# Optimization experiments

Measured on AMD Instinct MI355X. Metric: run time of the kernel, lower is better.

Reference implementation:

```python
import jax, jax.numpy as jnp
import numpy as np

WS = 8        # window_size
NH = 8        # num_heads
LN_EPS = 1e-5

# static relative-position index table [WS*WS, WS*WS], values in [0, (2*WS-1)**2)
def _rel_index(ws):
    coords = np.arange(ws)
    grid = np.stack(np.meshgrid(coords, coords, indexing='ij')).reshape(2, -1)  # [2, W2]
    rel = grid[:, :, None] - grid[:, None, :]            # [2, W2, W2]
    rel = rel.transpose(1, 2, 0).copy()                   # [W2, W2, 2]
    rel[..., 0] += ws - 1
    rel[..., 1] += ws - 1
    rel[..., 0] *= 2 * ws - 1
    return rel.sum(-1)                                    # [W2, W2]

REL_IDX = jnp.asarray(_rel_index(WS))


def _ln(x):
    # LayerNorm without affine params (elementwise_affine=False)
    mu = jnp.mean(x, axis=-1, keepdims=True)
    var = jnp.var(x, axis=-1, keepdims=True)
    return (x - mu) * jax.lax.rsqrt(var + LN_EPS)


def setup_inputs() -> dict:
    key = jax.random.key(0)
    ks = jax.random.split(key, 16)
    B, Hg, Wg, C = 8, 64, 64, 256
    L = Hg * Wg
    s = 0.02
    inp = {
        'x': jax.random.normal(ks[0], (B, L, C), jnp.float32),
        't_embed': jax.random.normal(ks[1], (B, C), jnp.float32),
        'H': Hg,
        'W': Wg,
        'adaln1_w': s * jax.random.normal(ks[2], (C, 2 * C), jnp.float32),
        'adaln1_b': jnp.zeros((2 * C,), jnp.float32),
        'adaln2_w': s * jax.random.normal(ks[3], (C, 2 * C), jnp.float32),
        'adaln2_b': jnp.zeros((2 * C,), jnp.float32),
        'bias_table': s * jax.random.normal(ks[4], ((2 * WS - 1) ** 2, NH), jnp.float32),
        'q_w': s * jax.random.normal(ks[5], (C, C), jnp.float32),
        'q_b': jnp.zeros((C,), jnp.float32),
        'k_w': s * jax.random.normal(ks[6], (C, C), jnp.float32),
        'k_b': jnp.zeros((C,), jnp.float32),
        'v_w': s * jax.random.normal(ks[7], (C, C), jnp.float32),
        'v_b': jnp.zeros((C,), jnp.float32),
        'o_w': s * jax.random.normal(ks[8], (C, C), jnp.float32),
        'o_b': jnp.zeros((C,), jnp.float32),
        'ffn1_w': s * jax.random.normal(ks[9], (C, 4 * C), jnp.float32),
        'ffn1_b': jnp.zeros((4 * C,), jnp.float32),
        'ffn2_w': s * jax.random.normal(ks[10], (4 * C, C), jnp.float32),
        'ffn2_b': jnp.zeros((C,), jnp.float32),
    }
    return inp


def reference(x, t_embed, H, W, adaln1_w, adaln1_b, adaln2_w, adaln2_b,
              bias_table, q_w, q_b, k_w, k_b, v_w, v_b, o_w, o_b,
              ffn1_w, ffn1_b, ffn2_w, ffn2_b):
    B, L, C = x.shape
    d = C // NH
    W2 = WS * WS
    sh = WS // 2  # cyclic shift (shifted=True)

    # --- AdaLN1 ---
    ss = t_embed @ adaln1_w + adaln1_b              # [B, 2C]
    scale, shift = jnp.split(ss, 2, axis=-1)
    xn = _ln(x) * (1.0 + scale[:, None, :]) + shift[:, None, :]

    # --- shifted window partition ---
    xg = xn.reshape(B, H, W, C)
    xg = jnp.roll(xg, (-sh, -sh), axis=(1, 2))
    xw = xg.reshape(B, H // WS, WS, W // WS, WS, C).transpose(0, 1, 3, 2, 4, 5)
    xw = xw.reshape(-1, W2, C)                       # [nwB, W2, C]
    nwB = xw.shape[0]

    # --- window attention with relative position bias ---
    q = (xw @ q_w + q_b).reshape(nwB, W2, NH, d).transpose(0, 2, 1, 3)
    k = (xw @ k_w + k_b).reshape(nwB, W2, NH, d).transpose(0, 2, 1, 3)
    v = (xw @ v_w + v_b).reshape(nwB, W2, NH, d).transpose(0, 2, 1, 3)
    logits = jnp.einsum('whqd,whkd->whqk', q, k) * (d ** -0.5)
    bias = bias_table[REL_IDX.reshape(-1)].reshape(W2, W2, NH).transpose(2, 0, 1)
    logits = logits + bias[None].astype(logits.dtype)
    attn = jax.nn.softmax(logits, axis=-1)
    out = jnp.einsum('whqk,whkd->whqd', attn, v).transpose(0, 2, 1, 3).reshape(nwB, W2, C)
    out = out @ o_w + o_b

    # --- window reverse + unshift ---
    xm = out.reshape(B, H // WS, W // WS, WS, WS, C).transpose(0, 1, 3, 2, 4, 5)
    xm = xm.reshape(B, H, W, C)
    xm = jnp.roll(xm, (sh, sh), axis=(1, 2))
    x = x + xm.reshape(B, L, C)

    # --- AdaLN2 + FFN (GELU exact, matching torch nn.GELU) ---
    ss2 = t_embed @ adaln2_w + adaln2_b
    sc2, sh2 = jnp.split(ss2, 2, axis=-1)
    xn2 = _ln(x) * (1.0 + sc2[:, None, :]) + sh2[:, None, :]
    h = jax.nn.gelu(xn2 @ ffn1_w + ffn1_b, approximate=False)
    x = x + (h @ ffn2_w + ffn2_b)
    return x
```

## Files before the change

kernel.cpp:

```cpp
#include <hip/hip_runtime.h>
#include <math.h>

#define WS_ 8
#define NH_ 8
#define C_ 256
#define B_ 8
#define M_ 32768
#define SH_ 4
#define LN_EPS 1e-5f
#define SL_ 8388608

typedef __attribute__((ext_vector_type(8))) short bf16x8;
typedef __attribute__((ext_vector_type(4))) float f32x4;

__device__ inline float b2f(unsigned short u) {
    union { unsigned int i; float f; } c; c.i = ((unsigned int)u) << 16; return c.f;
}
__device__ inline unsigned short f2b(float f) {
    union { unsigned int i; float f; } c; c.f = f;
    unsigned int u = c.i;
    return (unsigned short)((u + 0x7FFFu + ((u >> 16) & 1u)) >> 16);
}
__device__ inline float gelu_f(float x) {
    float t = 1.59576912160573f * (x + 0.044715f * x * x * x);
    return x / (1.f + __expf(-t));
}

__global__ void prep_k(const float* __restrict__ qw, const float* __restrict__ kw,
                       const float* __restrict__ vw, const float* __restrict__ ow,
                       const float* __restrict__ f1w, const float* __restrict__ f2w,
                       const float* __restrict__ qb, const float* __restrict__ kb,
                       const float* __restrict__ vb, const float* __restrict__ bt,
                       const float* __restrict__ te,
                       const float* __restrict__ a1w, const float* __restrict__ a1b,
                       const float* __restrict__ a2w, const float* __restrict__ a2b,
                       unsigned short* __restrict__ qkvT, unsigned short* __restrict__ oT,
                       unsigned short* __restrict__ f1T, unsigned short* __restrict__ f2T,
                       float* __restrict__ qkvB, float* __restrict__ bias_full,
                       float* __restrict__ ss1, float* __restrict__ ss2) {
    int t = blockIdx.x * 256 + threadIdx.x;
    if (t < 196608) {
        int n = t >> 8, k = t & 255;
        const float* w = n < 256 ? qw : (n < 512 ? kw : vw);
        qkvT[t] = f2b(w[k * 256 + (n & 255)]);
    } else if (t < 262144) {
        int i = t - 196608; int n = i >> 8, k = i & 255;
        oT[i] = f2b(ow[k * 256 + n]);
    } else if (t < 524288) {
        int i = t - 262144; int n = i >> 8, k = i & 255;
        f1T[i] = f2b(f1w[k * 1024 + n]);
    } else if (t < 786432) {
        int i = t - 524288; int n = i >> 10, k = i & 1023;
        f2T[i] = f2b(f2w[k * 256 + n]);
    } else if (t < 787200) {
        int i = t - 786432;
        qkvB[i] = i < 256 ? qb[i] : (i < 512 ? kb[i - 256] : vb[i - 512]);
    } else if (t < 819968) {
        int i = t - 787200;
        int head = i >> 12, qk = i & 4095;
        int q = qk >> 6, k = qk & 63;
        int qh = q >> 3, qw2 = q & 7, kh = k >> 3, kw2 = k & 7;
        bias_full[i] = bt[((qh - kh + 7) * 15 + (qw2 - kw2 + 7)) * 8 + head];
    } else if (t < 828160) {
        int i = t - 819968;
        int which = i >> 12;
        int rem = i & 4095;
        int b = rem >> 9, col = rem & 511;
        const float* w = which ? a2w : a1w;
        const float* bb = which ? a2b : a1b;
        const float* tr = te + b * C_;
        float acc = bb[col];
        for (int k = 0; k < C_; ++k) acc += tr[k] * w[k * 512 + col];
        (which ? ss2 : ss1)[b * 512 + col] = acc;
    }
}

__global__ __launch_bounds__(256) void ln_win_k(const float* __restrict__ x,
                                                const float* __restrict__ ss,
                                                unsigned short* __restrict__ xw) {
    int t = blockIdx.x * 4 + (threadIdx.x >> 6);
    int lane = threadIdx.x & 63;
    int b = t >> 12, rem = t & 4095;
    int hg = rem >> 6, wg = rem & 63;
    int hs = (hg + SH_) & 63, wsrc = (wg + SH_) & 63;
    size_t src = ((size_t)b << 12) + (hs << 6) + wsrc;
    float4 v = *(const float4*)&x[src * C_ + lane * 4];
    float s = v.x + v.y + v.z + v.w;
    float s2 = v.x * v.x + v.y * v.y + v.z * v.z + v.w * v.w;
#pragma unroll
    for (int m = 1; m < 64; m <<= 1) { s += __shfl_xor(s, m); s2 += __shfl_xor(s2, m); }
    float mu = s * (1.f / 256.f);
    float rstd = rsqrtf(s2 * (1.f / 256.f) - mu * mu + LN_EPS);
    float4 sc = *(const float4*)&ss[b * 512 + lane * 4];
    float4 sh = *(const float4*)&ss[b * 512 + 256 + lane * 4];
    int win = (b << 6) + ((hg >> 3) << 3) + (wg >> 3);
    int pos = ((hg & 7) << 3) + (wg & 7);
    ushort4 pk;
    pk.x = f2b((v.x - mu) * rstd * (1.f + sc.x) + sh.x);
    pk.y = f2b((v.y - mu) * rstd * (1.f + sc.y) + sh.y);
    pk.z = f2b((v.z - mu) * rstd * (1.f + sc.z) + sh.z);
    pk.w = f2b((v.w - mu) * rstd * (1.f + sc.w) + sh.w);
    *(ushort4*)(xw + (size_t)(win * 64 + pos) * C_ + lane * 4) = pk;
}

template <int KDIM, int MODE, int NT, int MINW>
__global__ __launch_bounds__(256, MINW) void gemm_bf16_k(
    const unsigned short* __restrict__ A, const unsigned short* __restrict__ Bt,
    const float* __restrict__ bias, const float* __restrict__ res,
    void* __restrict__ Cout, int Nout) {
    __shared__ __align__(16) unsigned short smem[16384];
    unsigned short (*As)[4096] = (unsigned short (*)[4096])&smem[0];
    unsigned short (*Bs)[4096] = (unsigned short (*)[4096])&smem[8192];
    const int blk = blockIdx.x;
    const int xcd = blk & 7;
    const int idx = blk >> 3;
    const int mt = xcd + ((idx / NT) << 3);
    const int nt = idx % NT;
    const int bm = mt * 128, bn = nt * 128;
    const int tid = threadIdx.x;
    const int w = tid >> 6, lane = tid & 63;
    const int quad = lane >> 4, l16 = lane & 15;
    const int wm = (w >> 1) * 64, wn = (w & 1) * 64;
    const int srow = lane >> 2;
    const int qlog = ((lane & 3) ^ ((lane >> 3) & 3)) << 3;
    const int rsw = ((l16 >> 1) & 3) << 3;

    f32x4 acc[4][4] = {};

    for (int k0 = 0; k0 < KDIM; k0 += 64) {
        if (k0) __syncthreads();
#pragma unroll
        for (int h = 0; h < 2; ++h) {
#pragma unroll
            for (int j = 0; j < 2; ++j) {
                int r = j * 64 + w * 16 + srow;
                const unsigned short* ga = A + (size_t)(bm + r) * KDIM + k0 + h * 32 + qlog;
                unsigned short* la = &As[h][j * 2048 + w * 512 + lane * 8];
                __builtin_amdgcn_global_load_lds(
                    (const __attribute__((address_space(1))) void*)ga,
                    (__attribute__((address_space(3))) void*)la, 16, 0, 0);
                const unsigned short* gb = Bt + (size_t)(bn + r) * KDIM + k0 + h * 32 + qlog;
                unsigned short* lb = &Bs[h][j * 2048 + w * 512 + lane * 8];
                __builtin_amdgcn_global_load_lds(
                    (const __attribute__((address_space(1))) void*)gb,
                    (__attribute__((address_space(3))) void*)lb, 16, 0, 0);
            }
        }
        __syncthreads();
#pragma unroll
        for (int h = 0; h < 2; ++h) {
            bf16x8 af[4], bfr[4];
#pragma unroll
            for (int i = 0; i < 4; ++i)
                af[i] = *(const bf16x8*)&As[h][(wm + i * 16 + l16) * 32 + ((quad << 3) ^ rsw)];
#pragma unroll
            for (int j = 0; j < 4; ++j)
                bfr[j] = *(const bf16x8*)&Bs[h][(wn + j * 16 + l16) * 32 + ((quad << 3) ^ rsw)];
#pragma unroll
            for (int i = 0; i < 4; ++i)
#pragma unroll
                for (int j = 0; j < 4; ++j)
                    acc[i][j] = __builtin_amdgcn_mfma_f32_16x16x32_bf16(
                        bfr[j], af[i], acc[i][j], 0, 0, 0);
        }
    }

    if constexpr (MODE == 0 || MODE == 2) {
        __syncthreads();
#pragma unroll
        for (int i = 0; i < 4; ++i) {
            const int lrow = wm + i * 16 + l16;
#pragma unroll
            for (int j = 0; j < 4; ++j) {
                const int lcol = wn + j * 16 + quad * 4;
                float4 bv = *(const float4*)&bias[bn + lcol];
                float v0 = acc[i][j][0] + bv.x, v1 = acc[i][j][1] + bv.y;
                float v2 = acc[i][j][2] + bv.z, v3 = acc[i][j][3] + bv.w;
                ushort4 pk;
                if (MODE == 2) {
                    pk.x = f2b(gelu_f(v0)); pk.y = f2b(gelu_f(v1));
                    pk.z = f2b(gelu_f(v2)); pk.w = f2b(gelu_f(v3));
                } else {
                    pk.x = f2b(v0); pk.y = f2b(v1); pk.z = f2b(v2); pk.w = f2b(v3);
                }
                int sw = (lcol >> 3) ^ (lrow & 7);
                *(ushort4*)&smem[lrow * 128 + sw * 8 + (lcol & 7)] = pk;
            }
        }
        __syncthreads();
#pragma unroll
        for (int p = 0; p < 8; ++p) {
            const int lrow = p * 16 + (tid >> 4);
            const int c16 = tid & 15;
            bf16x8 v = *(const bf16x8*)&smem[lrow * 128 + ((c16 ^ (lrow & 7)) * 8)];
            const int grow = bm + lrow;
            if (MODE == 2) {
                *(bf16x8*)((unsigned short*)Cout + (size_t)grow * Nout + bn + c16 * 8) = v;
            } else {
                int win = grow >> 6, pos = grow & 63;
                int col = bn + c16 * 8;
                int which = col >> 8, head = (col >> 5) & 7, dc = col & 31;
                *(bf16x8*)((unsigned short*)Cout + (size_t)which * SL_ +
                           (size_t)win * 16384 + pos * 32 + head * 2048 + dc) = v;
            }
        }
    } else {
#pragma unroll
        for (int i = 0; i < 4; ++i) {
            const int row = bm + wm + i * 16 + l16;
            size_t rowbase = (size_t)row * Nout;
#pragma unroll
            for (int j = 0; j < 4; ++j) {
                const int col = bn + wn + j * 16 + quad * 4;
                float4 bv = *(const float4*)&bias[col];
                float v0 = acc[i][j][0] + bv.x, v1 = acc[i][j][1] + bv.y;
                float v2 = acc[i][j][2] + bv.z, v3 = acc[i][j][3] + bv.w;
                float4 rv = *(const float4*)&res[rowbase + col];
                float4 ov = {v0 + rv.x, v1 + rv.y, v2 + rv.z, v3 + rv.w};
                *(float4*)&((float*)Cout)[rowbase + col] = ov;
            }
        }
    }
}

__global__ __launch_bounds__(512, 2) void oproj_ln_k(
    const unsigned short* __restrict__ A, const unsigned short* __restrict__ Bt,
    const float* __restrict__ bias, const float* __restrict__ res,
    float* __restrict__ x1, const float* __restrict__ ss2,
    unsigned short* __restrict__ xn2) {
    __shared__ __align__(16) unsigned short As[4][128 * 32];
    __shared__ __align__(16) unsigned short Bs[4][256 * 32];
    const int bm = blockIdx.x * 128;
    const int tid = threadIdx.x;
    const int w = tid >> 6, lane = tid & 63;
    const int quad = lane >> 4, l16 = lane & 15;
    const int wrow = (w >> 2) * 64, wcol = (w & 3) * 64;
    const int rsw = ((l16 >> 1) & 3) << 3;
    const int srow = tid >> 2;
    const int gch = ((tid & 3) ^ ((srow >> 1) & 3)) << 3;

    f32x4 acc[4][4] = {};

    for (int k0 = 0; k0 < 256; k0 += 128) {
        if (k0) __syncthreads();
#pragma unroll
        for (int h = 0; h < 4; ++h) {
            const unsigned short* ga = A + (size_t)(bm + srow) * 256 + k0 + h * 32 + gch;
            __builtin_amdgcn_global_load_lds(
                (const __attribute__((address_space(1))) void*)ga,
                (__attribute__((address_space(3))) void*)&As[h][tid * 8], 16, 0, 0);
#pragma unroll
            for (int s = 0; s < 2; ++s) {
                const unsigned short* gb = Bt + (size_t)(s * 128 + srow) * 256 + k0 + h * 32 + gch;
                __builtin_amdgcn_global_load_lds(
                    (const __attribute__((address_space(1))) void*)gb,
                    (__attribute__((address_space(3))) void*)&Bs[h][s * 4096 + tid * 8], 16, 0, 0);
            }
        }
        __syncthreads();
#pragma unroll
        for (int h = 0; h < 4; ++h) {
            bf16x8 af[4], bfr[4];
#pragma unroll
            for (int i = 0; i < 4; ++i)
                af[i] = *(const bf16x8*)&As[h][(wrow + i * 16 + l16) * 32 + ((quad << 3) ^ rsw)];
#pragma unroll
            for (int j = 0; j < 4; ++j)
                bfr[j] = *(const bf16x8*)&Bs[h][(wcol + j * 16 + l16) * 32 + ((quad << 3) ^ rsw)];
#pragma unroll
            for (int i = 0; i < 4; ++i)
#pragma unroll
                for (int j = 0; j < 4; ++j)
                    acc[i][j] = __builtin_amdgcn_mfma_f32_16x16x32_bf16(
                        bfr[j], af[i], acc[i][j], 0, 0, 0);
        }
    }

    float ps[4], ps2[4];
#pragma unroll
    for (int i = 0; i < 4; ++i) {
        const int row = bm + wrow + i * 16 + l16;
        int win = row >> 6, pos = row & 63;
        int b = win >> 6, wh = (win >> 3) & 7, ww = win & 7;
        int hg = (wh << 3) + (pos >> 3), wg = (ww << 3) + (pos & 7);
        int hd = (hg + SH_) & 63, wd = (wg + SH_) & 63;
        size_t rowbase = (((size_t)b << 12) + (hd << 6) + wd) * C_;
        float s = 0.f, s2 = 0.f;
#pragma unroll
        for (int j = 0; j < 4; ++j) {
            const int col = wcol + j * 16 + quad * 4;
            float4 bv = *(const float4*)&bias[col];
            float4 rv = *(const float4*)&res[rowbase + col];
            float4 ov = {acc[i][j][0] + bv.x + rv.x, acc[i][j][1] + bv.y + rv.y,
                         acc[i][j][2] + bv.z + rv.z, acc[i][j][3] + bv.w + rv.w};
            *(float4*)&x1[rowbase + col] = ov;
            acc[i][j][0] = ov.x; acc[i][j][1] = ov.y;
            acc[i][j][2] = ov.z; acc[i][j][3] = ov.w;
            s += ov.x + ov.y + ov.z + ov.w;
            s2 += ov.x * ov.x + ov.y * ov.y + ov.z * ov.z + ov.w * ov.w;
        }
        ps[i] = s; ps2[i] = s2;
    }
#pragma unroll
    for (int i = 0; i < 4; ++i) {
        ps[i] += __shfl_xor(ps[i], 16);  ps[i] += __shfl_xor(ps[i], 32);
        ps2[i] += __shfl_xor(ps2[i], 16); ps2[i] += __shfl_xor(ps2[i], 32);
    }
    float* sred = (float*)&As[0][0];
    __syncthreads();
    if (quad == 0) {
#pragma unroll
        for (int i = 0; i < 4; ++i) {
            int r = i * 16 + l16;
            sred[(w * 64 + r) * 2 + 0] = ps[i];
            sred[(w * 64 + r) * 2 + 1] = ps2[i];
        }
    }
    __syncthreads();
#pragma unroll
    for (int i = 0; i < 4; ++i) {
        int r = i * 16 + l16;
        float s = 0.f, s2 = 0.f;
#pragma unroll
        for (int cw = 0; cw < 4; ++cw) {
            s  += sred[(((w >> 2) * 4 + cw) * 64 + r) * 2 + 0];
            s2 += sred[(((w >> 2) * 4 + cw) * 64 + r) * 2 + 1];
        }
        float mu = s * (1.f / 256.f);
        float rstd = rsqrtf(s2 * (1.f / 256.f) - mu * mu + LN_EPS);
        const int row = bm + wrow + i * 16 + l16;
        int win = row >> 6, pos = row & 63;
        int b = win >> 6, wh = (win >> 3) & 7, ww = win & 7;
        int hg = (wh << 3) + (pos >> 3), wg = (ww << 3) + (pos & 7);
        int hd = (hg + SH_) & 63, wd = (wg + SH_) & 63;
        size_t rowbase = (((size_t)b << 12) + (hd << 6) + wd) * C_;
#pragma unroll
        for (int j = 0; j < 4; ++j) {
            const int col = wcol + j * 16 + quad * 4;
            float4 scv = *(const float4*)&ss2[b * 512 + col];
            float4 shv = *(const float4*)&ss2[b * 512 + 256 + col];
            ushort4 pk;
            pk.x = f2b((acc[i][j][0] - mu) * rstd * (1.f + scv.x) + shv.x);
            pk.y = f2b((acc[i][j][1] - mu) * rstd * (1.f + scv.y) + shv.y);
            pk.z = f2b((acc[i][j][2] - mu) * rstd * (1.f + scv.z) + shv.z);
            pk.w = f2b((acc[i][j][3] - mu) * rstd * (1.f + scv.w) + shv.w);
            *(ushort4*)(xn2 + rowbase + col) = pk;
        }
    }
}

__global__ __launch_bounds__(256) void attn_mfma_k(
    const unsigned short* __restrict__ qkv, const float* __restrict__ bias_full,
    unsigned short* __restrict__ attn_out) {
    __shared__ __align__(16) unsigned short Pb[4][64 * 66];
    __shared__ __align__(16) unsigned short Vt[4][32 * 66];
    const int w = threadIdx.x >> 6, lane = threadIdx.x & 63;
    const int wh = blockIdx.x * 4 + w;
    const int win = wh >> 3, head = wh & 7;
    const int quad = lane >> 4, l16 = lane & 15;

    const unsigned short* qp = qkv + (size_t)win * 16384 + head * 2048;
    const unsigned short* kp = qp + SL_;
    const unsigned short* vp = qp + 2 * (size_t)SL_;

    {
        const uint4* v4 = (const uint4*)(vp + lane * 32);
        unsigned short* dst = &Vt[w][0];
#pragma unroll
        for (int c = 0; c < 4; ++c) {
            uint4 u = v4[c];
            unsigned int uu[4] = {u.x, u.y, u.z, u.w};
#pragma unroll
            for (int p = 0; p < 4; ++p) {
                int d0 = c * 8 + p * 2;
                dst[d0 * 66 + lane] = (unsigned short)(uu[p] & 0xffff);
                dst[(d0 + 1) * 66 + lane] = (unsigned short)(uu[p] >> 16);
            }
        }
    }

    bf16x8 qf[4], kf[4];
#pragma unroll
    for (int i = 0; i < 4; ++i) {
        qf[i] = *(const bf16x8*)(qp + (i * 16 + l16) * 32 + quad * 8);
        kf[i] = *(const bf16x8*)(kp + (i * 16 + l16) * 32 + quad * 8);
    }

    f32x4 s[4][4] = {};
#pragma unroll
    for (int i = 0; i < 4; ++i)
#pragma unroll
        for (int j = 0; j < 4; ++j)
            s[i][j] = __builtin_amdgcn_mfma_f32_16x16x32_bf16(qf[i], kf[j], s[i][j], 0, 0, 0);

    const float scale = 0.17677669529663687f;
    const float* bf = bias_full + head * 4096;
    float rs[4][4];
#pragma unroll
    for (int i = 0; i < 4; ++i) {
#pragma unroll
        for (int r = 0; r < 4; ++r) {
            int row = i * 16 + quad * 4 + r;
            float acc = 0.f;
#pragma unroll
            for (int j = 0; j < 4; ++j) {
                float e = __expf(s[i][j][r] * scale + bf[row * 64 + j * 16 + l16]);
                s[i][j][r] = e;
                acc += e;
            }
#pragma unroll
            for (int msk = 1; msk < 16; msk <<= 1) acc += __shfl_xor(acc, msk);
            rs[i][r] = 1.f / acc;
        }
    }

#pragma unroll
    for (int i = 0; i < 4; ++i)
#pragma unroll
        for (int j = 0; j < 4; ++j)
#pragma unroll
            for (int r = 0; r < 4; ++r)
                Pb[w][(i * 16 + quad * 4 + r) * 66 + j * 16 + l16] = f2b(s[i][j][r]);

    __syncthreads();

    f32x4 o[4][2] = {};
#pragma unroll
    for (int st = 0; st < 2; ++st) {
        bf16x8 bv[2];
#pragma unroll
        for (int jo = 0; jo < 2; ++jo)
            bv[jo] = *(const bf16x8*)&Vt[w][(jo * 16 + l16) * 66 + st * 32 + quad * 8];
#pragma unroll
        for (int i = 0; i < 4; ++i) {
            bf16x8 af = *(const bf16x8*)&Pb[w][(i * 16 + l16) * 66 + st * 32 + quad * 8];
#pragma unroll
            for (int jo = 0; jo < 2; ++jo)
                o[i][jo] = __builtin_amdgcn_mfma_f32_16x16x32_bf16(af, bv[jo], o[i][jo], 0, 0, 0);
        }
    }

#pragma unroll
    for (int i = 0; i < 4; ++i)
#pragma unroll
        for (int jo = 0; jo < 2; ++jo)
#pragma unroll
            for (int r = 0; r < 4; ++r) {
                int row = i * 16 + quad * 4 + r;
                int d = jo * 16 + l16;
                attn_out[((size_t)(win * 64 + row)) * C_ + head * 32 + d] =
                    f2b(o[i][jo][r] * rs[i][r]);
            }
}

extern "C" void kernel_launch(void* const* d_in, const int* in_sizes, int n_in,
                              void* d_out, int out_size, void* d_ws, size_t ws_size,
                              hipStream_t stream) {
    const float* x        = (const float*)d_in[0];
    const float* t_embed  = (const float*)d_in[1];
    const float* adaln1_w = (const float*)d_in[4];
    const float* adaln1_b = (const float*)d_in[5];
    const float* adaln2_w = (const float*)d_in[6];
    const float* adaln2_b = (const float*)d_in[7];
    const float* bt       = (const float*)d_in[8];
    const float* q_w = (const float*)d_in[9],  *q_b = (const float*)d_in[10];
    const float* k_w = (const float*)d_in[11], *k_b = (const float*)d_in[12];
    const float* v_w = (const float*)d_in[13], *v_b = (const float*)d_in[14];
    const float* o_w = (const float*)d_in[15], *o_b = (const float*)d_in[16];
    const float* f1_w = (const float*)d_in[17], *f1_b = (const float*)d_in[18];
    const float* f2_w = (const float*)d_in[19], *f2_b = (const float*)d_in[20];
    float* out = (float*)d_out;

    char* wsb = (char*)d_ws;
    float* ss1            = (float*)(wsb + 0);
    float* ss2            = (float*)(wsb + 16384);
    float* qkvB           = (float*)(wsb + 32768);
    unsigned short* qkvT  = (unsigned short*)(wsb + 36864);
    unsigned short* oT    = (unsigned short*)(wsb + 430080);
    unsigned short* f1T   = (unsigned short*)(wsb + 561152);
    unsigned short* f2T   = (unsigned short*)(wsb + 1085440);
    float* bias_full      = (float*)(wsb + 1609728);
    unsigned short* xw    = (unsigned short*)(wsb + 2097152);
    unsigned short* qkv   = (unsigned short*)(wsb + 18874368);
    unsigned short* attn  = (unsigned short*)(wsb + 69206016);
    unsigned short* xn2   = xw;
    unsigned short* hbuf  = qkv;
    float* x1             = (float*)(wsb + 85983232);

    prep_k<<<3235, 256, 0, stream>>>(q_w, k_w, v_w, o_w, f1_w, f2_w, q_b, k_b, v_b, bt,
                                     t_embed, adaln1_w, adaln1_b, adaln2_w, adaln2_b,
                                     qkvT, oT, f1T, f2T, qkvB, bias_full, ss1, ss2);
    ln_win_k<<<8192, 256, 0, stream>>>(x, ss1, xw);

    gemm_bf16_k<256, 0, 6, 3><<<1536, 256, 0, stream>>>(xw, qkvT, qkvB, nullptr, qkv, 768);

    attn_mfma_k<<<1024, 256, 0, stream>>>(qkv, bias_full, attn);

    oproj_ln_k<<<256, 512, 0, stream>>>(attn, oT, o_b, x, x1, ss2, xn2);

    gemm_bf16_k<256, 2, 8, 3><<<2048, 256, 0, stream>>>(xn2, f1T, f1_b, nullptr, hbuf, 1024);
    gemm_bf16_k<1024, 3, 2, 1><<<512, 256, 0, stream>>>(hbuf, f2T, f2_b, x1, out, 256);
}
```

Before: 261.9 us.

## Fuse FFN1, GELU and FFN2 into one kernel keeping hidden activations in LDS

Replaces the two FFN GEMM launches with one kernel. Each block takes a 64-row tile and computes the hidden layer in four 256-wide chunks. Each chunk goes through GELU into swizzled shared memory and is consumed right away by the second GEMM, accumulating in registers. This removes the round trip of the 32768x1024 bf16 hidden tensor through global memory and one launch. In exchange, B weight fragments are read straight from global or L2 without LDS staging, and only 512 blocks are launched, which may limit occupancy.

New measurement: 268.6 us. 1.03x slower.

```diff
diff --git a/kernel.cpp b/kernel.cpp
--- a/kernel.cpp
+++ b/kernel.cpp
@@ -349,6 +349,113 @@
     }
 }
 
+__global__ __launch_bounds__(512, 4) void ffn_fused_k(
+    const unsigned short* __restrict__ xn2, const unsigned short* __restrict__ f1T,
+    const unsigned short* __restrict__ f2T, const float* __restrict__ f1b,
+    const float* __restrict__ f2bias, const float* __restrict__ x1,
+    float* __restrict__ out) {
+    __shared__ __align__(16) unsigned short Ahs[8][2048];
+    __shared__ __align__(16) unsigned short hs[64 * 256];
+    const int tid = threadIdx.x;
+    const int w = tid >> 6, lane = tid & 63;
+    const int quad = lane >> 4, l16 = lane & 15;
+    const int brow = blockIdx.x * 64;
+    const int rsw = ((l16 >> 1) & 3) << 3;
+
+    if (tid < 256) {
+        const int arow = tid >> 2;
+        const int qa = ((tid & 3) ^ ((tid >> 3) & 3)) << 3;
+#pragma unroll
+        for (int h = 0; h < 8; ++h) {
+            const unsigned short* ga = xn2 + (size_t)(brow + arow) * 256 + h * 32 + qa;
+            __builtin_amdgcn_global_load_lds(
+                (const __attribute__((address_space(1))) void*)ga,
+                (__attribute__((address_space(3))) void*)&Ahs[h][tid * 8], 16, 0, 0);
+        }
+    }
+    f32x4 acc2[4][2] = {};
+    __syncthreads();
+
+    for (int c = 0; c < 4; ++c) {
+        f32x4 a1[4][2] = {};
+        const unsigned short* bp1 =
+            f1T + (size_t)(c * 256 + w * 32 + l16) * 256 + quad * 8;
+#pragma unroll
+        for (int k8 = 0; k8 < 8; ++k8) {
+            bf16x8 ax[4], bf[2];
+#pragma unroll
+            for (int j = 0; j < 2; ++j)
+                bf[j] = *(const bf16x8*)(bp1 + (size_t)j * 16 * 256 + k8 * 32);
+#pragma unroll
+            for (int i = 0; i < 4; ++i)
+                ax[i] = *(const bf16x8*)&Ahs[k8][(i * 16 + l16) * 32 + ((quad << 3) ^ rsw)];
+            __builtin_amdgcn_s_setprio(1);
+#pragma unroll
+            for (int i = 0; i < 4; ++i)
+#pragma unroll
+                for (int j = 0; j < 2; ++j)
+                    a1[i][j] = __builtin_amdgcn_mfma_f32_16x16x32_bf16(
+                        bf[j], ax[i], a1[i][j], 0, 0, 0);
+            __builtin_amdgcn_s_setprio(0);
+        }
+        if (c) __syncthreads();
+#pragma unroll
+        for (int i = 0; i < 4; ++i) {
+            int row = i * 16 + l16;
+#pragma unroll
+            for (int j = 0; j < 2; ++j) {
+                int hl = w * 32 + j * 16 + quad * 4;
+                float4 bv = *(const float4*)&f1b[c * 256 + hl];
+                ushort4 pk;
+                pk.x = f2b(gelu_f(a1[i][j][0] + bv.x));
+                pk.y = f2b(gelu_f(a1[i][j][1] + bv.y));
+                pk.z = f2b(gelu_f(a1[i][j][2] + bv.z));
+                pk.w = f2b(gelu_f(a1[i][j][3] + bv.w));
+                int ch = hl >> 3, half = (hl >> 2) & 1;
+                *(ushort4*)&hs[row * 256 + ((ch ^ (row & 7)) << 3) + half * 4] = pk;
+            }
+        }
+        __syncthreads();
+        const unsigned short* bp2 =
+            f2T + (size_t)(w * 32 + l16) * 1024 + c * 256 + quad * 8;
+#pragma unroll
+        for (int k8 = 0; k8 < 8; ++k8) {
+            bf16x8 ah[4], bg[2];
+#pragma unroll
+            for (int jo = 0; jo < 2; ++jo)
+                bg[jo] = *(const bf16x8*)(bp2 + (size_t)jo * 16 * 1024 + k8 * 32);
+#pragma unroll
+            for (int i = 0; i < 4; ++i) {
+                int row = i * 16 + l16;
+                int ch = (k8 * 4 + quad) ^ (row & 7);
+                ah[i] = *(const bf16x8*)&hs[row * 256 + ch * 8];
+            }
+            __builtin_amdgcn_s_setprio(1);
+#pragma unroll
+            for (int i = 0; i < 4; ++i)
+#pragma unroll
+                for (int jo = 0; jo < 2; ++jo)
+                    acc2[i][jo] = __builtin_amdgcn_mfma_f32_16x16x32_bf16(
+                        bg[jo], ah[i], acc2[i][jo], 0, 0, 0);
+            __builtin_amdgcn_s_setprio(0);
+        }
+    }
+
+#pragma unroll
+    for (int i = 0; i < 4; ++i) {
+        int row = brow + i * 16 + l16;
+#pragma unroll
+        for (int jo = 0; jo < 2; ++jo) {
+            int col = w * 32 + jo * 16 + quad * 4;
+            float4 bv = *(const float4*)&f2bias[col];
+            float4 rv = *(const float4*)&x1[(size_t)row * 256 + col];
+            float4 ov = {acc2[i][jo][0] + bv.x + rv.x, acc2[i][jo][1] + bv.y + rv.y,
+                         acc2[i][jo][2] + bv.z + rv.z, acc2[i][jo][3] + bv.w + rv.w};
+            *(float4*)&out[(size_t)row * 256 + col] = ov;
+        }
+    }
+}
+
 __global__ __launch_bounds__(256) void attn_mfma_k(
     const unsigned short* __restrict__ qkv, const float* __restrict__ bias_full,
     unsigned short* __restrict__ attn_out) {
@@ -484,7 +591,6 @@
     unsigned short* qkv   = (unsigned short*)(wsb + 18874368);
     unsigned short* attn  = (unsigned short*)(wsb + 69206016);
     unsigned short* xn2   = xw;
-    unsigned short* hbuf  = qkv;
     float* x1             = (float*)(wsb + 85983232);
 
     prep_k<<<3235, 256, 0, stream>>>(q_w, k_w, v_w, o_w, f1_w, f2_w, q_b, k_b, v_b, bt,
@@ -498,6 +604,5 @@
 
     oproj_ln_k<<<256, 512, 0, stream>>>(attn, oT, o_b, x, x1, ss2, xn2);
 
-    gemm_bf16_k<256, 2, 8, 3><<<2048, 256, 0, stream>>>(xn2, f1T, f1_b, nullptr, hbuf, 1024);
-    gemm_bf16_k<1024, 3, 2, 1><<<512, 256, 0, stream>>>(hbuf, f2T, f2_b, x1, out, 256);
-}
+    ffn_fused_k<<<512, 512, 0, stream>>>(xn2, f1T, f2T, f1_b, f2_b, x1, out);
+}
```

## Keep full-K A tile resident in LDS across multiple N tiles for QKV and FFN1 GEMMs

Applied to the files above, without the earlier changes.

Adds a new GEMM kernel that loads a 128x256 A tile into LDS once and sweeps several 128-wide N tiles, streaming only B in 64-wide K slices. It replaces the QKV and FFN1 GEMM launches, cutting repeated global reads of A and launching fewer, larger (512-thread) blocks. The epilogue stages output through LDS for coalesced writes. The trade-offs are 80KB of LDS per block, which lowers occupancy, and a load/sync per K slice with no double buffering.

After: 264.6 us. About the same (+1.0%).

```diff
diff --git a/kernel.cpp b/kernel.cpp
--- a/kernel.cpp
+++ b/kernel.cpp
@@ -103,6 +103,124 @@
     *(ushort4*)(xw + (size_t)(win * 64 + pos) * C_ + lane * 4) = pk;
 }
 
+template <int MODE, int NTB>
+__global__ __launch_bounds__(512, 4) void gemm_pa_k(
+    const unsigned short* __restrict__ A, const unsigned short* __restrict__ Bt,
+    const float* __restrict__ bias, void* __restrict__ Cout, int Nout) {
+    __shared__ __align__(16) unsigned short As[128 * 256];
+    __shared__ __align__(16) unsigned short Bs[128 * 64];
+    const int blk = blockIdx.x;
+    const int mt = blk >> 1, ng = blk & 1;
+    const int bm = mt * 128;
+    const int tid = threadIdx.x;
+    const int w = tid >> 6, lane = tid & 63;
+    const int quad = lane >> 4, l16 = lane & 15;
+    const int wrow = (w >> 2) * 64;
+    const int wcol = (w & 3) * 32;
+
+    {
+#pragma unroll
+        for (int i = 0; i < 8; ++i) {
+            int r = w * 16 + 2 * i + (lane >> 5);
+            int p = lane & 31;
+            const unsigned short* ga =
+                A + (size_t)(bm + r) * 256 + ((p ^ (r & 7)) << 3);
+            __builtin_amdgcn_global_load_lds(
+                (const __attribute__((address_space(1))) void*)ga,
+                (__attribute__((address_space(3))) void*)
+                    &As[(w * 16 + 2 * i) * 256 + lane * 8], 16, 0, 0);
+        }
+    }
+
+    for (int nt = 0; nt < NTB; ++nt) {
+        const int bn = (ng * NTB + nt) * 128;
+        f32x4 acc[4][2] = {};
+#pragma unroll
+        for (int ks = 0; ks < 4; ++ks) {
+            __syncthreads();
+#pragma unroll
+            for (int s = 0; s < 2; ++s) {
+                int r = w * 16 + s * 8 + (lane >> 3);
+                int p = lane & 7;
+                const unsigned short* gb = Bt + (size_t)(bn + r) * 256 +
+                                           ks * 64 + ((p ^ (r & 7)) << 3);
+                __builtin_amdgcn_global_load_lds(
+                    (const __attribute__((address_space(1))) void*)gb,
+                    (__attribute__((address_space(3))) void*)
+                        &Bs[(w * 16 + s * 8) * 64 + lane * 8], 16, 0, 0);
+            }
+            __syncthreads();
+#pragma unroll
+            for (int h = 0; h < 2; ++h) {
+                bf16x8 af[4], bf[2];
+#pragma unroll
+                for (int i = 0; i < 4; ++i) {
+                    int ra = wrow + i * 16 + l16;
+                    int cc = ks * 8 + h * 4 + quad;
+                    af[i] = *(const bf16x8*)&As[ra * 256 + ((cc ^ (ra & 7)) << 3)];
+                }
+#pragma unroll
+                for (int j = 0; j < 2; ++j) {
+                    int rb = wcol + j * 16 + l16;
+                    int cl = h * 4 + quad;
+                    bf[j] = *(const bf16x8*)&Bs[rb * 64 + ((cl ^ (rb & 7)) << 3)];
+                }
+#pragma unroll
+                for (int i = 0; i < 4; ++i)
+#pragma unroll
+                    for (int j = 0; j < 2; ++j)
+                        acc[i][j] = __builtin_amdgcn_mfma_f32_16x16x32_bf16(
+                            bf[j], af[i], acc[i][j], 0, 0, 0);
+            }
+        }
+#pragma unroll
+        for (int half = 0; half < 2; ++half) {
+            __syncthreads();
+            if ((w >> 2) == half) {
+#pragma unroll
+                for (int i = 0; i < 4; ++i) {
+                    int lr = i * 16 + l16;
+#pragma unroll
+                    for (int j = 0; j < 2; ++j) {
+                        int lc = wcol + j * 16 + quad * 4;
+                        float4 bv = *(const float4*)&bias[bn + lc];
+                        float v0 = acc[i][j][0] + bv.x, v1 = acc[i][j][1] + bv.y;
+                        float v2 = acc[i][j][2] + bv.z, v3 = acc[i][j][3] + bv.w;
+                        ushort4 pk;
+                        if (MODE == 2) {
+                            pk.x = f2b(gelu_f(v0)); pk.y = f2b(gelu_f(v1));
+                            pk.z = f2b(gelu_f(v2)); pk.w = f2b(gelu_f(v3));
+                        } else {
+                            pk.x = f2b(v0); pk.y = f2b(v1);
+                            pk.z = f2b(v2); pk.w = f2b(v3);
+                        }
+                        int sw = (lc >> 3) ^ (lr & 7);
+                        *(ushort4*)&Bs[lr * 128 + sw * 8 + (lc & 7)] = pk;
+                    }
+                }
+            }
+            __syncthreads();
+#pragma unroll
+            for (int s = 0; s < 2; ++s) {
+                int idx = s * 512 + tid;
+                int lr = idx >> 4, c16 = idx & 15;
+                bf16x8 v = *(const bf16x8*)&Bs[lr * 128 + ((c16 ^ (lr & 7)) * 8)];
+                int grow = bm + half * 64 + lr;
+                if (MODE == 2) {
+                    *(bf16x8*)((unsigned short*)Cout + (size_t)grow * Nout +
+                               bn + c16 * 8) = v;
+                } else {
+                    int win = grow >> 6, pos = grow & 63;
+                    int col = bn + c16 * 8;
+                    int which = col >> 8, head = (col >> 5) & 7, dc = col & 31;
+                    *(bf16x8*)((unsigned short*)Cout + (size_t)which * SL_ +
+                               (size_t)win * 16384 + pos * 32 + head * 2048 + dc) = v;
+                }
+            }
+        }
+    }
+}
+
 template <int KDIM, int MODE, int NT, int MINW>
 __global__ __launch_bounds__(256, MINW) void gemm_bf16_k(
     const unsigned short* __restrict__ A, const unsigned short* __restrict__ Bt,
@@ -492,12 +610,12 @@
                                      qkvT, oT, f1T, f2T, qkvB, bias_full, ss1, ss2);
     ln_win_k<<<8192, 256, 0, stream>>>(x, ss1, xw);
 
-    gemm_bf16_k<256, 0, 6, 3><<<1536, 256, 0, stream>>>(xw, qkvT, qkvB, nullptr, qkv, 768);
+    gemm_pa_k<0, 3><<<512, 512, 0, stream>>>(xw, qkvT, qkvB, qkv, 768);
 
     attn_mfma_k<<<1024, 256, 0, stream>>>(qkv, bias_full, attn);
 
     oproj_ln_k<<<256, 512, 0, stream>>>(attn, oT, o_b, x, x1, ss2, xn2);
 
-    gemm_bf16_k<256, 2, 8, 3><<<2048, 256, 0, stream>>>(xn2, f1T, f1_b, nullptr, hbuf, 1024);
+    gemm_pa_k<2, 4><<<512, 512, 0, stream>>>(xn2, f1T, f1_b, hbuf, 1024);
     gemm_bf16_k<1024, 3, 2, 1><<<512, 256, 0, stream>>>(hbuf, f2T, f2_b, x1, out, 256);
 }
```

## Load GEMM B operand directly from global, halve LDS, retile oproj for occupancy

Applied to the files above, without the earlier changes.

The generic bf16 GEMM stops staging the weight (B) tile in shared memory and has each lane read its B fragments straight from global memory (weights should sit in cache). This halves LDS use, and the epilogue is split into two 64-row halves so the smaller buffer still works. The o-proj+LayerNorm kernel is retiled from 128 rows by 512 threads to 64 rows by 256 threads, and launch-bounds minimum occupancy rises to 4 blocks per CU. This trades LDS traffic and barrier cost for higher occupancy, but adds uncoalesced, latency-exposed global loads in the inner loop plus an extra barrier round in the epilogue.

After: 316.7 us. 1.21x slower.

```diff
diff --git a/kernel.cpp b/kernel.cpp
--- a/kernel.cpp
+++ b/kernel.cpp
@@ -108,9 +108,7 @@
     const unsigned short* __restrict__ A, const unsigned short* __restrict__ Bt,
     const float* __restrict__ bias, const float* __restrict__ res,
     void* __restrict__ Cout, int Nout) {
-    __shared__ __align__(16) unsigned short smem[16384];
-    unsigned short (*As)[4096] = (unsigned short (*)[4096])&smem[0];
-    unsigned short (*Bs)[4096] = (unsigned short (*)[4096])&smem[8192];
+    __shared__ __align__(16) unsigned short As[2][4096];
     const int blk = blockIdx.x;
     const int xcd = blk & 7;
     const int idx = blk >> 3;
@@ -126,6 +124,7 @@
     const int rsw = ((l16 >> 1) & 3) << 3;
 
     f32x4 acc[4][4] = {};
+    const unsigned short* bp = Bt + (size_t)(bn + wn + l16) * KDIM + quad * 8;
 
     for (int k0 = 0; k0 < KDIM; k0 += 64) {
         if (k0) __syncthreads();
@@ -139,11 +138,6 @@
                 __builtin_amdgcn_global_load_lds(
                     (const __attribute__((address_space(1))) void*)ga,
                     (__attribute__((address_space(3))) void*)la, 16, 0, 0);
-                const unsigned short* gb = Bt + (size_t)(bn + r) * KDIM + k0 + h * 32 + qlog;
-                unsigned short* lb = &Bs[h][j * 2048 + w * 512 + lane * 8];
-                __builtin_amdgcn_global_load_lds(
-                    (const __attribute__((address_space(1))) void*)gb,
-                    (__attribute__((address_space(3))) void*)lb, 16, 0, 0);
             }
         }
         __syncthreads();
@@ -151,11 +145,11 @@
         for (int h = 0; h < 2; ++h) {
             bf16x8 af[4], bfr[4];
 #pragma unroll
+            for (int j = 0; j < 4; ++j)
+                bfr[j] = *(const bf16x8*)(bp + (size_t)j * 16 * KDIM + k0 + h * 32);
+#pragma unroll
             for (int i = 0; i < 4; ++i)
                 af[i] = *(const bf16x8*)&As[h][(wm + i * 16 + l16) * 32 + ((quad << 3) ^ rsw)];
-#pragma unroll
-            for (int j = 0; j < 4; ++j)
-                bfr[j] = *(const bf16x8*)&Bs[h][(wn + j * 16 + l16) * 32 + ((quad << 3) ^ rsw)];
 #pragma unroll
             for (int i = 0; i < 4; ++i)
 #pragma unroll
@@ -166,42 +160,50 @@
     }
 
     if constexpr (MODE == 0 || MODE == 2) {
-        __syncthreads();
-#pragma unroll
-        for (int i = 0; i < 4; ++i) {
-            const int lrow = wm + i * 16 + l16;
-#pragma unroll
-            for (int j = 0; j < 4; ++j) {
-                const int lcol = wn + j * 16 + quad * 4;
-                float4 bv = *(const float4*)&bias[bn + lcol];
-                float v0 = acc[i][j][0] + bv.x, v1 = acc[i][j][1] + bv.y;
-                float v2 = acc[i][j][2] + bv.z, v3 = acc[i][j][3] + bv.w;
-                ushort4 pk;
+        unsigned short* bb = &As[0][0];
+#pragma unroll
+        for (int half = 0; half < 2; ++half) {
+            __syncthreads();
+            if ((w >> 1) == half) {
+#pragma unroll
+                for (int i = 0; i < 4; ++i) {
+                    const int lr = i * 16 + l16;
+#pragma unroll
+                    for (int j = 0; j < 4; ++j) {
+                        const int lc = wn + j * 16 + quad * 4;
+                        float4 bv = *(const float4*)&bias[bn + lc];
+                        float v0 = acc[i][j][0] + bv.x, v1 = acc[i][j][1] + bv.y;
+                        float v2 = acc[i][j][2] + bv.z, v3 = acc[i][j][3] + bv.w;
+                        ushort4 pk;
+                        if (MODE == 2) {
+                            pk.x = f2b(gelu_f(v0)); pk.y = f2b(gelu_f(v1));
+                            pk.z = f2b(gelu_f(v2)); pk.w = f2b(gelu_f(v3));
+                        } else {
+                            pk.x = f2b(v0); pk.y = f2b(v1);
+                            pk.z = f2b(v2); pk.w = f2b(v3);
+                        }
+                        int sw = (lc >> 3) ^ (lr & 7);
+                        *(ushort4*)&bb[lr * 128 + sw * 8 + (lc & 7)] = pk;
+                    }
+                }
+            }
+            __syncthreads();
+#pragma unroll
+            for (int s = 0; s < 4; ++s) {
+                int iidx = s * 256 + tid;
+                int lr = iidx >> 4, c16 = iidx & 15;
+                bf16x8 v = *(const bf16x8*)&bb[lr * 128 + ((c16 ^ (lr & 7)) * 8)];
+                const int grow = bm + half * 64 + lr;
                 if (MODE == 2) {
-                    pk.x = f2b(gelu_f(v0)); pk.y = f2b(gelu_f(v1));
-                    pk.z = f2b(gelu_f(v2)); pk.w = f2b(gelu_f(v3));
+                    *(bf16x8*)((unsigned short*)Cout + (size_t)grow * Nout +
+                               bn + c16 * 8) = v;
                 } else {
-                    pk.x = f2b(v0); pk.y = f2b(v1); pk.z = f2b(v2); pk.w = f2b(v3);
+                    int win = grow >> 6, pos = grow & 63;
+                    int col = bn + c16 * 8;
+                    int which = col >> 8, head = (col >> 5) & 7, dc = col & 31;
+                    *(bf16x8*)((unsigned short*)Cout + (size_t)which * SL_ +
+                               (size_t)win * 16384 + pos * 32 + head * 2048 + dc) = v;
                 }
-                int sw = (lcol >> 3) ^ (lrow & 7);
-                *(ushort4*)&smem[lrow * 128 + sw * 8 + (lcol & 7)] = pk;
-            }
-        }
-        __syncthreads();
-#pragma unroll
-        for (int p = 0; p < 8; ++p) {
-            const int lrow = p * 16 + (tid >> 4);
-            const int c16 = tid & 15;
-            bf16x8 v = *(const bf16x8*)&smem[lrow * 128 + ((c16 ^ (lrow & 7)) * 8)];
-            const int grow = bm + lrow;
-            if (MODE == 2) {
-                *(bf16x8*)((unsigned short*)Cout + (size_t)grow * Nout + bn + c16 * 8) = v;
-            } else {
-                int win = grow >> 6, pos = grow & 63;
-                int col = bn + c16 * 8;
-                int which = col >> 8, head = (col >> 5) & 7, dc = col & 31;
-                *(bf16x8*)((unsigned short*)Cout + (size_t)which * SL_ +
-                           (size_t)win * 16384 + pos * 32 + head * 2048 + dc) = v;
             }
         }
     } else {
@@ -223,50 +225,56 @@
     }
 }
 
-__global__ __launch_bounds__(512, 2) void oproj_ln_k(
+__global__ __launch_bounds__(256, 4) void oproj_ln_k(
     const unsigned short* __restrict__ A, const unsigned short* __restrict__ Bt,
     const float* __restrict__ bias, const float* __restrict__ res,
     float* __restrict__ x1, const float* __restrict__ ss2,
     unsigned short* __restrict__ xn2) {
-    __shared__ __align__(16) unsigned short As[4][128 * 32];
-    __shared__ __align__(16) unsigned short Bs[4][256 * 32];
-    const int bm = blockIdx.x * 128;
+    __shared__ __align__(16) unsigned short As[2][64 * 32];
+    __shared__ __align__(16) unsigned short Bs[2][256 * 32];
+    const int bm = blockIdx.x * 64;
     const int tid = threadIdx.x;
     const int w = tid >> 6, lane = tid & 63;
     const int quad = lane >> 4, l16 = lane & 15;
-    const int wrow = (w >> 2) * 64, wcol = (w & 3) * 64;
+    const int wn = w * 64;
+    const int srow = lane >> 2;
+    const int qlog = ((lane & 3) ^ ((lane >> 3) & 3)) << 3;
     const int rsw = ((l16 >> 1) & 3) << 3;
-    const int srow = tid >> 2;
-    const int gch = ((tid & 3) ^ ((srow >> 1) & 3)) << 3;
 
     f32x4 acc[4][4] = {};
 
-    for (int k0 = 0; k0 < 256; k0 += 128) {
+    for (int k0 = 0; k0 < 256; k0 += 64) {
         if (k0) __syncthreads();
 #pragma unroll
-        for (int h = 0; h < 4; ++h) {
-            const unsigned short* ga = A + (size_t)(bm + srow) * 256 + k0 + h * 32 + gch;
-            __builtin_amdgcn_global_load_lds(
-                (const __attribute__((address_space(1))) void*)ga,
-                (__attribute__((address_space(3))) void*)&As[h][tid * 8], 16, 0, 0);
-#pragma unroll
-            for (int s = 0; s < 2; ++s) {
-                const unsigned short* gb = Bt + (size_t)(s * 128 + srow) * 256 + k0 + h * 32 + gch;
+        for (int h = 0; h < 2; ++h) {
+            {
+                int r = w * 16 + srow;
+                const unsigned short* ga = A + (size_t)(bm + r) * 256 + k0 + h * 32 + qlog;
+                __builtin_amdgcn_global_load_lds(
+                    (const __attribute__((address_space(1))) void*)ga,
+                    (__attribute__((address_space(3))) void*)&As[h][w * 512 + lane * 8],
+                    16, 0, 0);
+            }
+#pragma unroll
+            for (int j = 0; j < 4; ++j) {
+                int r = j * 64 + w * 16 + srow;
+                const unsigned short* gb = Bt + (size_t)r * 256 + k0 + h * 32 + qlog;
                 __builtin_amdgcn_global_load_lds(
                     (const __attribute__((address_space(1))) void*)gb,
-                    (__attribute__((address_space(3))) void*)&Bs[h][s * 4096 + tid * 8], 16, 0, 0);
+                    (__attribute__((address_space(3))) void*)
+                        &Bs[h][j * 2048 + w * 512 + lane * 8], 16, 0, 0);
             }
         }
         __syncthreads();
 #pragma unroll
-        for (int h = 0; h < 4; ++h) {
+        for (int h = 0; h < 2; ++h) {
             bf16x8 af[4], bfr[4];
 #pragma unroll
             for (int i = 0; i < 4; ++i)
-                af[i] = *(const bf16x8*)&As[h][(wrow + i * 16 + l16) * 32 + ((quad << 3) ^ rsw)];
+                af[i] = *(const bf16x8*)&As[h][(i * 16 + l16) * 32 + ((quad << 3) ^ rsw)];
 #pragma unroll
             for (int j = 0; j < 4; ++j)
-                bfr[j] = *(const bf16x8*)&Bs[h][(wcol + j * 16 + l16) * 32 + ((quad << 3) ^ rsw)];
+                bfr[j] = *(const bf16x8*)&Bs[h][(wn + j * 16 + l16) * 32 + ((quad << 3) ^ rsw)];
 #pragma unroll
             for (int i = 0; i < 4; ++i)
 #pragma unroll
@@ -279,7 +287,7 @@
     float ps[4], ps2[4];
 #pragma unroll
     for (int i = 0; i < 4; ++i) {
-        const int row = bm + wrow + i * 16 + l16;
+        const int row = bm + i * 16 + l16;
         int win = row >> 6, pos = row & 63;
         int b = win >> 6, wh = (win >> 3) & 7, ww = win & 7;
         int hg = (wh << 3) + (pos >> 3), wg = (ww << 3) + (pos & 7);
@@ -288,7 +296,7 @@
         float s = 0.f, s2 = 0.f;
 #pragma unroll
         for (int j = 0; j < 4; ++j) {
-            const int col = wcol + j * 16 + quad * 4;
+            const int col = wn + j * 16 + quad * 4;
             float4 bv = *(const float4*)&bias[col];
             float4 rv = *(const float4*)&res[rowbase + col];
             float4 ov = {acc[i][j][0] + bv.x + rv.x, acc[i][j][1] + bv.y + rv.y,
@@ -323,12 +331,12 @@
         float s = 0.f, s2 = 0.f;
 #pragma unroll
         for (int cw = 0; cw < 4; ++cw) {
-            s  += sred[(((w >> 2) * 4 + cw) * 64 + r) * 2 + 0];
-            s2 += sred[(((w >> 2) * 4 + cw) * 64 + r) * 2 + 1];
+            s  += sred[(cw * 64 + r) * 2 + 0];
+            s2 += sred[(cw * 64 + r) * 2 + 1];
         }
         float mu = s * (1.f / 256.f);
         float rstd = rsqrtf(s2 * (1.f / 256.f) - mu * mu + LN_EPS);
-        const int row = bm + wrow + i * 16 + l16;
+        const int row = bm + i * 16 + l16;
         int win = row >> 6, pos = row & 63;
         int b = win >> 6, wh = (win >> 3) & 7, ww = win & 7;
         int hg = (wh << 3) + (pos >> 3), wg = (ww << 3) + (pos & 7);
@@ -336,7 +344,7 @@
         size_t rowbase = (((size_t)b << 12) + (hd << 6) + wd) * C_;
 #pragma unroll
         for (int j = 0; j < 4; ++j) {
-            const int col = wcol + j * 16 + quad * 4;
+            const int col = wn + j * 16 + quad * 4;
             float4 scv = *(const float4*)&ss2[b * 512 + col];
             float4 shv = *(const float4*)&ss2[b * 512 + 256 + col];
             ushort4 pk;
@@ -492,12 +500,12 @@
                                      qkvT, oT, f1T, f2T, qkvB, bias_full, ss1, ss2);
     ln_win_k<<<8192, 256, 0, stream>>>(x, ss1, xw);
 
-    gemm_bf16_k<256, 0, 6, 3><<<1536, 256, 0, stream>>>(xw, qkvT, qkvB, nullptr, qkv, 768);
+    gemm_bf16_k<256, 0, 6, 4><<<1536, 256, 0, stream>>>(xw, qkvT, qkvB, nullptr, qkv, 768);
 
     attn_mfma_k<<<1024, 256, 0, stream>>>(qkv, bias_full, attn);
 
-    oproj_ln_k<<<256, 512, 0, stream>>>(attn, oT, o_b, x, x1, ss2, xn2);
-
-    gemm_bf16_k<256, 2, 8, 3><<<2048, 256, 0, stream>>>(xn2, f1T, f1_b, nullptr, hbuf, 1024);
-    gemm_bf16_k<1024, 3, 2, 1><<<512, 256, 0, stream>>>(hbuf, f2T, f2_b, x1, out, 256);
-}
+    oproj_ln_k<<<512, 256, 0, stream>>>(attn, oT, o_b, x, x1, ss2, xn2);
+
+    gemm_bf16_k<256, 2, 8, 4><<<2048, 256, 0, stream>>>(xn2, f1T, f1_b, nullptr, hbuf, 1024);
+    gemm_bf16_k<1024, 3, 2, 4><<<512, 256, 0, stream>>>(hbuf, f2T, f2_b, x1, out, 256);
+}
```
